# Kernel optimization log

Hardware: AMD Instinct MI355X
Metric: run time of the kernel (lower is better)

## Reference

```python
import jax, jax.numpy as jnp
import numpy as np


def _conv2d(x, w, b):
    # NCHW valid conv, kernel shape OIHW
    y = jax.lax.conv_general_dilated(x, w, (1, 1), 'VALID',
                                     dimension_numbers=('NCHW', 'OIHW', 'NCHW'))
    return y + b[None, :, None, None]


def _rgcn(x, src, dst, edge_type, root, rel, bias):
    # PyG RGCNConv: out_i = x_i @ root + bias + sum_r mean_{j in N_r(i)} x_j @ W_r
    # x: [B, N, F]; src/dst: [E]; rel: [R, F, F]
    out = x @ root + bias
    N = x.shape[1]
    for r in range(rel.shape[0]):  # small fixed relation count
        m = (edge_type == r).astype(x.dtype)                # [E]
        msg = (x @ rel[r])[:, src] * m[None, :, None]       # [B, E, F]
        agg = jnp.zeros_like(out).at[:, dst].add(msg)       # [B, N, F]
        cnt = jnp.zeros((N,), x.dtype).at[dst].add(m)       # per-node relation degree
        out = out + agg / jnp.clip(cnt, 1.0)[None, :, None]
    return out


def setup_inputs() -> dict:
    key = jax.random.key(0)
    ks = jax.random.split(key, 16)
    B, C, N, T = 16, 3, 3000, 50
    E, R, S, F = 96000, 3, 500, 43  # F = 2*20 + 3
    observation = jax.random.normal(ks[0], (B, C, N, T), jnp.float32)
    last_action = jax.random.uniform(ks[1], (B, S + 1), dtype=jnp.float32)
    edge_index = jax.random.randint(ks[2], (2, E), 0, N, jnp.int32)
    edge_type = jax.random.randint(ks[3], (E,), 0, R, jnp.int32)
    nodes_to_select = jnp.sort(jax.random.randint(ks[4], (S,), 0, N, jnp.int32))

    def w(k, shape, fan_in):
        return jax.random.normal(k, shape, jnp.float32) / np.sqrt(fan_in).astype(np.float32)

    params = dict(
        ws1=w(ks[5], (3, 3, 1, 3), 9), bs1=jnp.zeros(3, jnp.float32),
        ws2=w(ks[6], (20, 3, 1, 48), 144), bs2=jnp.zeros(20, jnp.float32),
        wm1=w(ks[7], (3, 3, 1, 21), 63), bm1=jnp.zeros(3, jnp.float32),
        wm2=w(ks[8], (20, 3, 1, 30), 90), bm2=jnp.zeros(20, jnp.float32),
        root1=w(ks[9], (F, F), F), rel1=w(ks[10], (R, F, F), F), bias1=jnp.zeros(F, jnp.float32),
        root2=w(ks[11], (F, F), F), rel2=w(ks[12], (R, F, F), F), bias2=jnp.zeros(F, jnp.float32),
        wf=w(ks[13], (1, 87, 1, 1), 87), bf=jnp.zeros(1, jnp.float32),
    )
    return {"observation": observation, "last_action": last_action,
            "edge_index": edge_index, "edge_type": edge_type,
            "nodes_to_select": nodes_to_select, **params}


def reference(observation, last_action, edge_index, edge_type, nodes_to_select,
              ws1, bs1, ws2, bs2, wm1, bm1, wm2, bm2,
              root1, rel1, bias1, root2, rel2, bias2, wf, bf):
    relu = jax.nn.relu
    B = observation.shape[0]
    last_stocks = last_action[:, 1:][:, None, :, None]                      # [B,1,S,1]
    short = relu(_conv2d(relu(_conv2d(observation, ws1, bs1)), ws2, bs2))   # [B,20,N,1]
    mid = relu(_conv2d(relu(_conv2d(observation, wm1, bm1)), wm2, bm2))     # [B,20,N,1]
    longf = relu(jnp.max(observation, axis=3, keepdims=True))               # [B,3,N,1]
    temporal = jnp.concatenate([short, mid, longf], axis=1)                 # [B,43,N,1]
    x = jnp.transpose(temporal[..., 0], (0, 2, 1))                          # [B,N,43]
    src, dst = edge_index[0], edge_index[1]
    h = jax.nn.leaky_relu(_rgcn(x, src, dst, edge_type, root1, rel1, bias1), 0.01)
    h = jax.nn.leaky_relu(_rgcn(h, src, dst, edge_type, root2, rel2, bias2), 0.01)
    graph_features = jnp.transpose(h, (0, 2, 1))[..., None]                 # [B,43,N,1]
    feats = jnp.concatenate([temporal, graph_features], axis=1)             # [B,86,N,1]
    feats = feats[:, :, nodes_to_select, :]                                 # [B,86,S,1]
    feats = jnp.concatenate([last_stocks, feats], axis=1)                   # [B,87,S,1]
    out = _conv2d(feats, wf, bf)                                            # [B,1,S,1]
    cash = jnp.zeros((B, 1, 1, 1), out.dtype)  # cash bias zeroed in mu()
    logits = jnp.concatenate([cash, out], axis=2)[:, 0, :, 0]               # [B,S+1]
    return jax.nn.softmax(logits, axis=-1)  # softmax_temperature = 1
```

## Files before the change

kernel.cpp:

```cpp
#include <hip/hip_runtime.h>
#include <math.h>

#define NB 16
#define NC 3
#define NN 3000
#define NT 50
#define NE 96000
#define NR 3
#define NS 500
#define NF 43
#define NFP 44
#define NBF (NB*NFP)
#define NBKT (NR*NN)
#define CAP 96

#define XT_OFF   0
#define H1_OFF   (XT_OFF + NN*NBF)
#define LG_OFF   (H1_OFF + NN*NBF)
#define INT_BASE (LG_OFF + NB*(NS+1))
#define CNT_OFF  0
#define EBUF_OFF (CNT_OFF + NBKT)

__global__ __launch_bounds__(256, 3) void k_front(
    const float* __restrict__ obs,
    const float* __restrict__ ws1, const float* __restrict__ bs1,
    const float* __restrict__ ws2, const float* __restrict__ bs2,
    const float* __restrict__ wm1, const float* __restrict__ bm1,
    const float* __restrict__ wm2, const float* __restrict__ bm2,
    float* __restrict__ x,
    const int* __restrict__ ei, const int* __restrict__ et,
    int* __restrict__ cnt, int* __restrict__ ebuf)
{
    __shared__ float sp[4][64][23];
    int tid = threadIdx.x;

    if (blockIdx.x >= 1500) {
        int e = (blockIdx.x - 1500) * 256 + tid;
        int bkt = et[e] * NN + ei[NE + e];
        int pos = atomicAdd(&cnt[bkt], 1);
        if (pos < CAP) ebuf[bkt * CAP + pos] = ei[e];
        return;
    }

    int wave = __builtin_amdgcn_readfirstlane(tid >> 6);
    int lane = tid & 63;

    if (blockIdx.x < 750) {
        int idx = blockIdx.x * 64 + lane;
        int b = idx / NN, n = idx - b * NN;
        float wS[3][14];
        int base = 12 * wave;
        #pragma unroll
        for (int c = 0; c < 3; ++c) {
            const float2* p2 = (const float2*)(obs + ((size_t)(b * NC + c) * NN + n) * NT + base);
            #pragma unroll
            for (int jj = 0; jj < 7; ++jj) {
                float2 u = p2[jj];
                wS[c][2 * jj] = u.x; wS[c][2 * jj + 1] = u.y;
            }
        }
        float acc[20];
        #pragma unroll
        for (int o = 0; o < 20; ++o) acc[o] = 0.f;
        #pragma unroll
        for (int j = 0; j < 12; ++j) {
            float y[3];
            #pragma unroll
            for (int c = 0; c < 3; ++c) {
                float s = bs1[c];
                #pragma unroll
                for (int i = 0; i < 3; ++i)
                    #pragma unroll
                    for (int k = 0; k < 3; ++k)
                        s = fmaf(wS[i][j + k], ws1[(c * 3 + i) * 3 + k], s);
                y[c] = fmaxf(s, 0.f);
            }
            int gt = base + j;
            #pragma unroll
            for (int o = 0; o < 20; ++o) {
                float a = acc[o];
                #pragma unroll
                for (int c = 0; c < 3; ++c)
                    a = fmaf(y[c], ws2[(o * 3 + c) * 48 + gt], a);
                acc[o] = a;
            }
        }
        #pragma unroll
        for (int o = 0; o < 20; ++o) sp[wave][lane][o] = acc[o];
        __syncthreads();
        #pragma unroll
        for (int q = 0; q < 5; ++q) {
            int item = q * 256 + tid;
            int node = item / 20, o = item - node * 20;
            int g = blockIdx.x * 64 + node;
            int bb = g / NN, nn = g - bb * NN;
            float s = ((sp[0][node][o] + sp[1][node][o]) +
                       (sp[2][node][o] + sp[3][node][o])) + bs2[o];
            x[(size_t)nn * NBF + bb * NFP + o] = fmaxf(s, 0.f);
        }
        return;
    }

    {
        int idx = (blockIdx.x - 750) * 64 + lane;
        int b = idx / NN, n = idx - b * NN;
        int mbase = (wave < 3) ? 8 * wave : 24;
        int nld   = (wave < 3) ? 14 : 13;
        const float* orow = obs + ((size_t)b * NC * NN + n) * NT + mbase;

        float s[3][8];
        #pragma unroll
        for (int c = 0; c < 3; ++c)
            #pragma unroll
            for (int t = 0; t < 8; ++t) s[c][t] = bm1[c];
        float cmax[3];
        float wA[28], wB[28];

        #define LOADW(buf, ch)                                                  \
        {                                                                       \
            const float2* p2 = (const float2*)(orow + (size_t)(ch) * NN * NT);  \
            _Pragma("unroll")                                                   \
            for (int jj = 0; jj < 14; ++jj) {                                   \
                if (jj < nld) {                                                 \
                    float2 u = p2[jj];                                          \
                    buf[2 * jj] = u.x; buf[2 * jj + 1] = u.y;                   \
                } else { buf[2 * jj] = 0.f; buf[2 * jj + 1] = 0.f; }            \
            }                                                                   \
        }
        #define COMPW(buf, ii)                                                  \
        {                                                                       \
            float m = buf[0];                                                   \
            _Pragma("unroll")                                                   \
            for (int t = 1; t < 28; ++t) m = fmaxf(m, buf[t]);                  \
            cmax[ii] = m;                                                       \
            _Pragma("unroll")                                                   \
            for (int c = 0; c < 3; ++c)                                         \
                _Pragma("unroll")                                               \
                for (int t = 0; t < 8; ++t) {                                   \
                    float a = s[c][t];                                          \
                    _Pragma("unroll")                                           \
                    for (int k = 0; k < 21; ++k)                                \
                        a = fmaf(buf[t + k], wm1[(c * 3 + (ii)) * 21 + k], a);  \
                    s[c][t] = a;                                                \
                }                                                               \
        }

        LOADW(wA, 0)
        LOADW(wB, 1)
        COMPW(wA, 0)
        LOADW(wA, 2)
        COMPW(wB, 1)
        COMPW(wA, 2)
        #undef LOADW
        #undef COMPW

        float acc[20];
        #pragma unroll
        for (int o = 0; o < 20; ++o) acc[o] = 0.f;
        int cntM = (wave < 3) ? 8 : 6;
        #pragma unroll
        for (int j = 0; j < 8; ++j) {
            if (j < cntM) {
                float y0 = fmaxf(s[0][j], 0.f);
                float y1 = fmaxf(s[1][j], 0.f);
                float y2 = fmaxf(s[2][j], 0.f);
                int gt = mbase + j;
                #pragma unroll
                for (int o = 0; o < 20; ++o) {
                    float a = acc[o];
                    a = fmaf(y0, wm2[(o * 3 + 0) * 30 + gt], a);
                    a = fmaf(y1, wm2[(o * 3 + 1) * 30 + gt], a);
                    a = fmaf(y2, wm2[(o * 3 + 2) * 30 + gt], a);
                    acc[o] = a;
                }
            }
        }
        #pragma unroll
        for (int o = 0; o < 20; ++o) sp[wave][lane][o] = acc[o];
        #pragma unroll
        for (int c = 0; c < 3; ++c) sp[wave][lane][20 + c] = cmax[c];
    }
    __syncthreads();
    #pragma unroll
    for (int q = 0; q < 6; ++q) {
        int item = q * 256 + tid;
        if (item < 1472) {
            int node = item / 23, o = item - node * 23;
            int g = (blockIdx.x - 750) * 64 + node;
            int bb = g / NN, nn = g - bb * NN;
            size_t row = (size_t)nn * NBF + bb * NFP;
            if (o < 20) {
                float s = ((sp[0][node][o] + sp[1][node][o]) +
                           (sp[2][node][o] + sp[3][node][o])) + bm2[o];
                x[row + 20 + o] = fmaxf(s, 0.f);
            } else {
                float m = fmaxf(fmaxf(sp[0][node][o], sp[1][node][o]),
                                fmaxf(sp[2][node][o], sp[3][node][o]));
                x[row + 40 + (o - 20)] = fmaxf(m, 0.f);
            }
        }
    }
}

template<bool LEAKY, bool SEL>
__global__ __launch_bounds__(256) void k_rgcn(
    const float* __restrict__ in, const float* __restrict__ xsrc,
    const int* __restrict__ cnt, const int* __restrict__ ebuf,
    const int* __restrict__ sel,
    const float* __restrict__ root, const float* __restrict__ rel,
    const float* __restrict__ bias,
    const float* __restrict__ la, const float* __restrict__ wf,
    const float* __restrict__ bf,
    float* __restrict__ out)
{
    __shared__ float lrow[4][NBF];
    __shared__ float sP[8][4][NFP];

    int tid = threadIdx.x;
    int wave = __builtin_amdgcn_readfirstlane(tid >> 6);
    int lane = tid & 63;
    int i = blockIdx.x;
    int node = __builtin_amdgcn_readfirstlane(SEL ? sel[i] : i);

    const float* wbase = (wave == 0) ? root : (rel + (size_t)(wave - 1) * NF * NF);
    float wsl[43];
    #pragma unroll
    for (int j = 0; j < 43; ++j)
        wsl[j] = (lane < NF) ? wbase[j * NF + lane] : 0.f;

    if (wave == 3) {
        #pragma unroll
        for (int j = 0; j < 11; ++j) {
            float v = in[(size_t)node * NBF + j * 64 + lane];
            if (LEAKY) v = v >= 0.f ? v : 0.01f * v;
            lrow[0][j * 64 + lane] = v;
        }
    } else {
        int bkt = wave * NN + node;
        int cvr = __builtin_amdgcn_readfirstlane(cnt[bkt]);
        float ic = 1.0f / fmaxf((float)cvr, 1.0f);
        int cv = cvr > CAP ? CAP : cvr;
        const int* eb = ebuf + bkt * CAP;

        float acc[11];
        #pragma unroll
        for (int j = 0; j < 11; ++j) acc[j] = 0.f;

        for (int e = 0; e < cv; e += 4) {
            int4 q = *(const int4*)(eb + e);
            int m = cv - e;
            {
                const float* p = in + (size_t)__builtin_amdgcn_readfirstlane(q.x) * NBF;
                #pragma unroll
                for (int j = 0; j < 11; ++j) {
                    float v = p[j * 64 + lane];
                    if (LEAKY) v = v >= 0.f ? v : 0.01f * v;
                    acc[j] += v;
                }
            }
            if (m > 1) {
                const float* p = in + (size_t)__builtin_amdgcn_readfirstlane(q.y) * NBF;
                #pragma unroll
                for (int j = 0; j < 11; ++j) {
                    float v = p[j * 64 + lane];
                    if (LEAKY) v = v >= 0.f ? v : 0.01f * v;
                    acc[j] += v;
                }
            }
            if (m > 2) {
                const float* p = in + (size_t)__builtin_amdgcn_readfirstlane(q.z) * NBF;
                #pragma unroll
                for (int j = 0; j < 11; ++j) {
                    float v = p[j * 64 + lane];
                    if (LEAKY) v = v >= 0.f ? v : 0.01f * v;
                    acc[j] += v;
                }
            }
            if (m > 3) {
                const float* p = in + (size_t)__builtin_amdgcn_readfirstlane(q.w) * NBF;
                #pragma unroll
                for (int j = 0; j < 11; ++j) {
                    float v = p[j * 64 + lane];
                    if (LEAKY) v = v >= 0.f ? v : 0.01f * v;
                    acc[j] += v;
                }
            }
        }
        #pragma unroll
        for (int j = 0; j < 11; ++j) lrow[wave + 1][j * 64 + lane] = acc[j] * ic;
    }
    __syncthreads();

    for (int h = 0; h < 2; ++h) {
        #pragma unroll
        for (int rr = 0; rr < 8; ++rr) {
            int b = h * 8 + rr;
            const float4* a4 = (const float4*)&lrow[wave][b * NFP];
            float a0 = 0.f, a1 = 0.f, a2 = 0.f, a3 = 0.f;
            #pragma unroll
            for (int c = 0; c < 10; ++c) {
                float4 v = a4[c];
                a0 = fmaf(v.x, wsl[4 * c], a0);
                a1 = fmaf(v.y, wsl[4 * c + 1], a1);
                a2 = fmaf(v.z, wsl[4 * c + 2], a2);
                a3 = fmaf(v.w, wsl[4 * c + 3], a3);
            }
            {
                float4 v = a4[10];
                a0 = fmaf(v.x, wsl[40], a0);
                a1 = fmaf(v.y, wsl[41], a1);
                a2 = fmaf(v.z, wsl[42], a2);
            }
            if (lane < NF) sP[rr][wave][lane] = (a0 + a1) + (a2 + a3);
        }
        __syncthreads();

        int r0 = 2 * wave, r1 = 2 * wave + 1;
        int b0 = h * 8 + r0, b1 = h * 8 + r1;
        if (!SEL) {
            if (lane < NF) {
                float bi_ = bias[lane];
                float s0 = ((sP[r0][0][lane] + sP[r0][1][lane]) +
                            (sP[r0][2][lane] + sP[r0][3][lane])) + bi_;
                float s1 = ((sP[r1][0][lane] + sP[r1][1][lane]) +
                            (sP[r1][2][lane] + sP[r1][3][lane])) + bi_;
                out[(size_t)i * NBF + b0 * NFP + lane] = s0;
                out[(size_t)i * NBF + b1 * NFP + lane] = s1;
            }
        } else {
            float p0 = 0.f, p1 = 0.f;
            if (lane < NF) {
                float bi_ = bias[lane];
                float s0 = ((sP[r0][0][lane] + sP[r0][1][lane]) +
                            (sP[r0][2][lane] + sP[r0][3][lane])) + bi_;
                float s1 = ((sP[r1][0][lane] + sP[r1][1][lane]) +
                            (sP[r1][2][lane] + sP[r1][3][lane])) + bi_;
                s0 = s0 >= 0.f ? s0 : 0.01f * s0;
                s1 = s1 >= 0.f ? s1 : 0.01f * s1;
                float x0 = xsrc[(size_t)node * NBF + b0 * NFP + lane];
                float x1 = xsrc[(size_t)node * NBF + b1 * NFP + lane];
                p0 = fmaf(wf[44 + lane], s0, wf[1 + lane] * x0);
                p1 = fmaf(wf[44 + lane], s1, wf[1 + lane] * x1);
            }
            #pragma unroll
            for (int o = 32; o > 0; o >>= 1) {
                p0 += __shfl_down(p0, o);
                p1 += __shfl_down(p1, o);
            }
            if (lane == 0) {
                out[(size_t)b0 * (NS + 1) + 1 + i] =
                    p0 + bf[0] + wf[0] * la[b0 * (NS + 1) + 1 + i];
                out[(size_t)b1 * (NS + 1) + 1 + i] =
                    p1 + bf[0] + wf[0] * la[b1 * (NS + 1) + 1 + i];
            }
        }
        __syncthreads();
    }
}

__device__ inline float wred_max(float v) {
    #pragma unroll
    for (int o = 32; o > 0; o >>= 1) v = fmaxf(v, __shfl_down(v, o));
    return v;
}
__device__ inline float wred_sum(float v) {
    #pragma unroll
    for (int o = 32; o > 0; o >>= 1) v += __shfl_down(v, o);
    return v;
}

__global__ __launch_bounds__(512) void k_softmax(
    const float* __restrict__ lg, float* __restrict__ out)
{
    __shared__ float sred[8];
    __shared__ float sbc[2];
    int b = blockIdx.x, tid = threadIdx.x;

    float val = -3.0e38f;
    if (tid <= NS) val = (tid == 0) ? 0.f : lg[(size_t)b * (NS + 1) + tid];

    float m = wred_max(val);
    if ((tid & 63) == 0) sred[tid >> 6] = m;
    __syncthreads();
    if (tid == 0) {
        float mm = sred[0];
        #pragma unroll
        for (int i = 1; i < 8; ++i) mm = fmaxf(mm, sred[i]);
        sbc[0] = mm;
    }
    __syncthreads();
    float mx = sbc[0];
    float e = (tid <= NS) ? expf(val - mx) : 0.f;
    float s = wred_sum(e);
    if ((tid & 63) == 0) sred[tid >> 6] = s;
    __syncthreads();
    if (tid == 0) {
        float t = 0.f;
        #pragma unroll
        for (int i = 0; i < 8; ++i) t += sred[i];
        sbc[1] = t;
    }
    __syncthreads();
    if (tid <= NS) out[(size_t)b * (NS + 1) + tid] = e / sbc[1];
}

extern "C" void kernel_launch(void* const* d_in, const int* in_sizes, int n_in,
                              void* d_out, int out_size, void* d_ws, size_t ws_size,
                              hipStream_t stream)
{
    const float* obs   = (const float*)d_in[0];
    const float* la    = (const float*)d_in[1];
    const int*   ei    = (const int*)d_in[2];
    const int*   et    = (const int*)d_in[3];
    const int*   nodes = (const int*)d_in[4];
    const float* ws1 = (const float*)d_in[5],  *bs1 = (const float*)d_in[6];
    const float* ws2 = (const float*)d_in[7],  *bs2 = (const float*)d_in[8];
    const float* wm1 = (const float*)d_in[9],  *bm1 = (const float*)d_in[10];
    const float* wm2 = (const float*)d_in[11], *bm2 = (const float*)d_in[12];
    const float* root1 = (const float*)d_in[13], *rel1 = (const float*)d_in[14], *bias1 = (const float*)d_in[15];
    const float* root2 = (const float*)d_in[16], *rel2 = (const float*)d_in[17], *bias2 = (const float*)d_in[18];
    const float* wf = (const float*)d_in[19], *bf = (const float*)d_in[20];

    float* wsp = (float*)d_ws;
    float* x   = wsp + XT_OFF;
    float* h1  = wsp + H1_OFF;
    float* lg  = wsp + LG_OFF;
    int*   ibase = (int*)(wsp + INT_BASE);
    int*   cnt   = ibase + CNT_OFF;
    int*   ebuf  = ibase + EBUF_OFF;

    hipMemsetAsync(cnt, 0, NBKT * sizeof(int), stream);

    k_front<<<1875, 256, 0, stream>>>(
        obs, ws1, bs1, ws2, bs2, wm1, bm1, wm2, bm2, x, ei, et, cnt, ebuf);

    k_rgcn<false, false><<<NN, 256, 0, stream>>>(
        x, nullptr, cnt, ebuf, nullptr, root1, rel1, bias1,
        nullptr, nullptr, nullptr, h1);

    k_rgcn<true, true><<<NS, 256, 0, stream>>>(
        h1, x, cnt, ebuf, nodes, root2, rel2, bias2,
        la, wf, bf, lg);

    k_softmax<<<NB, 512, 0, stream>>>(lg, (float*)d_out);
}
```

Measured before the change: 210.8 us.

## Stage observation tiles in LDS and spread edge gathers across all waves

The front kernel now loads each block's observation rows into shared memory with coalesced float2 loads, and the per-wave conv windows are read from there instead of from strided global rows. In the RGCN kernel all four waves now split every relation's neighbour list, striding by four and doing two gathers per iteration. Partial sums are combined with LDS atomics, and the mean normalisation is folded into the relation weight scale. This targets uncoalesced global loads and the load imbalance where one wave handled only the self row, at the cost of extra syncs, more LDS use and LDS atomic adds.

```diff
diff --git a/kernel.cpp b/kernel.cpp
--- a/kernel.cpp
+++ b/kernel.cpp
@@ -21,6 +21,8 @@
 #define CNT_OFF  0
 #define EBUF_OFF (CNT_OFF + NBKT)
 
+#define TS 51
+
 __global__ __launch_bounds__(256, 3) void k_front(
     const float* __restrict__ obs,
     const float* __restrict__ ws1, const float* __restrict__ bs1,
@@ -31,7 +33,7 @@
     const int* __restrict__ ei, const int* __restrict__ et,
     int* __restrict__ cnt, int* __restrict__ ebuf)
 {
-    __shared__ float sp[4][64][23];
+    __shared__ float smem[3 * 64 * TS];
     int tid = threadIdx.x;
 
     if (blockIdx.x >= 1500) {
@@ -44,21 +46,39 @@
 
     int wave = __builtin_amdgcn_readfirstlane(tid >> 6);
     int lane = tid & 63;
-
-    if (blockIdx.x < 750) {
-        int idx = blockIdx.x * 64 + lane;
-        int b = idx / NN, n = idx - b * NN;
+    bool isA = blockIdx.x < 750;
+    int idx0 = (isA ? blockIdx.x : blockIdx.x - 750) * 64;
+
+    #pragma unroll
+    for (int k = 0; k < 19; ++k) {
+        int f2 = k * 256 + tid;
+        if (f2 < 4800) {
+            int c = f2 / 1600;
+            int rem = f2 - c * 1600;
+            int nr = rem / 25;
+            int tp = rem - nr * 25;
+            int idx = idx0 + nr;
+            int b = idx / NN, n = idx - b * NN;
+            float2 u = *(const float2*)(obs + ((size_t)(b * NC + c) * NN + n) * NT + 2 * tp);
+            float* d = &smem[(c * 64 + nr) * TS + 2 * tp];
+            d[0] = u.x; d[1] = u.y;
+        }
+    }
+    __syncthreads();
+
+    #define SP(w, nd, o) smem[((w) * 64 + (nd)) * 23 + (o)]
+
+    if (isA) {
+        int base = 12 * wave;
         float wS[3][14];
-        int base = 12 * wave;
         #pragma unroll
         for (int c = 0; c < 3; ++c) {
-            const float2* p2 = (const float2*)(obs + ((size_t)(b * NC + c) * NN + n) * NT + base);
-            #pragma unroll
-            for (int jj = 0; jj < 7; ++jj) {
-                float2 u = p2[jj];
-                wS[c][2 * jj] = u.x; wS[c][2 * jj + 1] = u.y;
-            }
-        }
+            const float* sr = &smem[(c * 64 + lane) * TS + base];
+            #pragma unroll
+            for (int jj = 0; jj < 14; ++jj) wS[c][jj] = sr[jj];
+        }
+        __syncthreads();
+
         float acc[20];
         #pragma unroll
         for (int o = 0; o < 20; ++o) acc[o] = 0.f;
@@ -86,27 +106,24 @@
             }
         }
         #pragma unroll
-        for (int o = 0; o < 20; ++o) sp[wave][lane][o] = acc[o];
+        for (int o = 0; o < 20; ++o) SP(wave, lane, o) = acc[o];
         __syncthreads();
         #pragma unroll
         for (int q = 0; q < 5; ++q) {
             int item = q * 256 + tid;
             int node = item / 20, o = item - node * 20;
-            int g = blockIdx.x * 64 + node;
+            int g = idx0 + node;
             int bb = g / NN, nn = g - bb * NN;
-            float s = ((sp[0][node][o] + sp[1][node][o]) +
-                       (sp[2][node][o] + sp[3][node][o])) + bs2[o];
+            float s = ((SP(0, node, o) + SP(1, node, o)) +
+                       (SP(2, node, o) + SP(3, node, o))) + bs2[o];
             x[(size_t)nn * NBF + bb * NFP + o] = fmaxf(s, 0.f);
         }
         return;
     }
 
     {
-        int idx = (blockIdx.x - 750) * 64 + lane;
-        int b = idx / NN, n = idx - b * NN;
         int mbase = (wave < 3) ? 8 * wave : 24;
-        int nld   = (wave < 3) ? 14 : 13;
-        const float* orow = obs + ((size_t)b * NC * NN + n) * NT + mbase;
+        int nld   = (wave < 3) ? 28 : 26;
 
         float s[3][8];
         #pragma unroll
@@ -116,33 +133,29 @@
         float cmax[3];
         float wA[28], wB[28];
 
-        #define LOADW(buf, ch)                                                  \
-        {                                                                       \
-            const float2* p2 = (const float2*)(orow + (size_t)(ch) * NN * NT);  \
-            _Pragma("unroll")                                                   \
-            for (int jj = 0; jj < 14; ++jj) {                                   \
-                if (jj < nld) {                                                 \
-                    float2 u = p2[jj];                                          \
-                    buf[2 * jj] = u.x; buf[2 * jj + 1] = u.y;                   \
-                } else { buf[2 * jj] = 0.f; buf[2 * jj + 1] = 0.f; }            \
-            }                                                                   \
-        }
-        #define COMPW(buf, ii)                                                  \
-        {                                                                       \
-            float m = buf[0];                                                   \
-            _Pragma("unroll")                                                   \
-            for (int t = 1; t < 28; ++t) m = fmaxf(m, buf[t]);                  \
-            cmax[ii] = m;                                                       \
-            _Pragma("unroll")                                                   \
-            for (int c = 0; c < 3; ++c)                                         \
-                _Pragma("unroll")                                               \
-                for (int t = 0; t < 8; ++t) {                                   \
-                    float a = s[c][t];                                          \
-                    _Pragma("unroll")                                           \
-                    for (int k = 0; k < 21; ++k)                                \
-                        a = fmaf(buf[t + k], wm1[(c * 3 + (ii)) * 21 + k], a);  \
-                    s[c][t] = a;                                                \
-                }                                                               \
+        #define LOADW(buf, ch)                                              \
+        {                                                                   \
+            const float* sr = &smem[((ch) * 64 + lane) * TS + mbase];       \
+            _Pragma("unroll")                                               \
+            for (int t = 0; t < 28; ++t)                                    \
+                buf[t] = (t < nld) ? sr[t] : 0.f;                           \
+        }
+        #define COMPW(buf, ii)                                              \
+        {                                                                   \
+            float m = buf[0];                                               \
+            _Pragma("unroll")                                               \
+            for (int t = 1; t < 28; ++t) m = fmaxf(m, buf[t]);              \
+            cmax[ii] = m;                                                   \
+            _Pragma("unroll")                                               \
+            for (int c = 0; c < 3; ++c)                                     \
+                _Pragma("unroll")                                           \
+                for (int t = 0; t < 8; ++t) {                               \
+                    float a = s[c][t];                                      \
+                    _Pragma("unroll")                                       \
+                    for (int k = 0; k < 21; ++k)                            \
+                        a = fmaf(buf[t + k], wm1[(c * 3 + (ii)) * 21 + k], a); \
+                    s[c][t] = a;                                            \
+                }                                                           \
         }
 
         LOADW(wA, 0)
@@ -153,6 +166,7 @@
         COMPW(wA, 2)
         #undef LOADW
         #undef COMPW
+        __syncthreads();
 
         float acc[20];
         #pragma unroll
@@ -176,9 +190,9 @@
             }
         }
         #pragma unroll
-        for (int o = 0; o < 20; ++o) sp[wave][lane][o] = acc[o];
-        #pragma unroll
-        for (int c = 0; c < 3; ++c) sp[wave][lane][20 + c] = cmax[c];
+        for (int o = 0; o < 20; ++o) SP(wave, lane, o) = acc[o];
+        #pragma unroll
+        for (int c = 0; c < 3; ++c) SP(wave, lane, 20 + c) = cmax[c];
     }
     __syncthreads();
     #pragma unroll
@@ -186,20 +200,21 @@
         int item = q * 256 + tid;
         if (item < 1472) {
             int node = item / 23, o = item - node * 23;
-            int g = (blockIdx.x - 750) * 64 + node;
+            int g = idx0 + node;
             int bb = g / NN, nn = g - bb * NN;
             size_t row = (size_t)nn * NBF + bb * NFP;
             if (o < 20) {
-                float s = ((sp[0][node][o] + sp[1][node][o]) +
-                           (sp[2][node][o] + sp[3][node][o])) + bm2[o];
+                float s = ((SP(0, node, o) + SP(1, node, o)) +
+                           (SP(2, node, o) + SP(3, node, o))) + bm2[o];
                 x[row + 20 + o] = fmaxf(s, 0.f);
             } else {
-                float m = fmaxf(fmaxf(sp[0][node][o], sp[1][node][o]),
-                                fmaxf(sp[2][node][o], sp[3][node][o]));
+                float m = fmaxf(fmaxf(SP(0, node, o), SP(1, node, o)),
+                                fmaxf(SP(2, node, o), SP(3, node, o)));
                 x[row + 40 + (o - 20)] = fmaxf(m, 0.f);
             }
         }
     }
+    #undef SP
 }
 
 template<bool LEAKY, bool SEL>
@@ -222,73 +237,81 @@
     int i = blockIdx.x;
     int node = __builtin_amdgcn_readfirstlane(SEL ? sel[i] : i);
 
-    const float* wbase = (wave == 0) ? root : (rel + (size_t)(wave - 1) * NF * NF);
-    float wsl[43];
-    #pragma unroll
-    for (int j = 0; j < 43; ++j)
-        wsl[j] = (lane < NF) ? wbase[j * NF + lane] : 0.f;
-
-    if (wave == 3) {
-        #pragma unroll
-        for (int j = 0; j < 11; ++j) {
-            float v = in[(size_t)node * NBF + j * 64 + lane];
+    {
+        float* lz = &lrow[1][0];
+        #pragma unroll
+        for (int k = 0; k < 9; ++k) {
+            int t = k * 256 + tid;
+            if (t < 3 * NBF) lz[t] = 0.f;
+        }
+    }
+
+    int cv_[3]; float ic_[3];
+    #pragma unroll
+    for (int r = 0; r < 3; ++r) {
+        int c0 = __builtin_amdgcn_readfirstlane(cnt[r * NN + node]);
+        ic_[r] = 1.0f / fmaxf((float)c0, 1.0f);
+        cv_[r] = c0 > CAP ? CAP : c0;
+    }
+
+    #pragma unroll
+    for (int j = 0; j < 3; ++j) {
+        int sl = wave + 4 * j;
+        if (sl < 11) {
+            float v = in[(size_t)node * NBF + sl * 64 + lane];
             if (LEAKY) v = v >= 0.f ? v : 0.01f * v;
-            lrow[0][j * 64 + lane] = v;
-        }
-    } else {
-        int bkt = wave * NN + node;
-        int cvr = __builtin_amdgcn_readfirstlane(cnt[bkt]);
-        float ic = 1.0f / fmaxf((float)cvr, 1.0f);
-        int cv = cvr > CAP ? CAP : cvr;
-        const int* eb = ebuf + bkt * CAP;
-
-        float acc[11];
-        #pragma unroll
-        for (int j = 0; j < 11; ++j) acc[j] = 0.f;
-
-        for (int e = 0; e < cv; e += 4) {
-            int4 q = *(const int4*)(eb + e);
-            int m = cv - e;
-            {
-                const float* p = in + (size_t)__builtin_amdgcn_readfirstlane(q.x) * NBF;
+            lrow[0][sl * 64 + lane] = v;
+        }
+    }
+    __syncthreads();
+
+    #pragma unroll
+    for (int r = 0; r < 3; ++r) {
+        int cv = cv_[r];
+        if (cv > wave) {
+            const int* eb = ebuf + (size_t)(r * NN + node) * CAP;
+            float acc[11];
+            #pragma unroll
+            for (int j = 0; j < 11; ++j) acc[j] = 0.f;
+            int e = wave;
+            for (; e + 4 < cv; e += 8) {
+                int i0 = __builtin_amdgcn_readfirstlane(eb[e]);
+                int i1 = __builtin_amdgcn_readfirstlane(eb[e + 4]);
+                const float* p0 = in + (size_t)i0 * NBF;
+                const float* p1 = in + (size_t)i1 * NBF;
                 #pragma unroll
                 for (int j = 0; j < 11; ++j) {
-                    float v = p[j * 64 + lane];
+                    float va = p0[j * 64 + lane];
+                    float vb = p1[j * 64 + lane];
+                    if (LEAKY) {
+                        va = va >= 0.f ? va : 0.01f * va;
+                        vb = vb >= 0.f ? vb : 0.01f * vb;
+                    }
+                    acc[j] += va + vb;
+                }
+            }
+            if (e < cv) {
+                int i0 = __builtin_amdgcn_readfirstlane(eb[e]);
+                const float* p0 = in + (size_t)i0 * NBF;
+                #pragma unroll
+                for (int j = 0; j < 11; ++j) {
+                    float v = p0[j * 64 + lane];
                     if (LEAKY) v = v >= 0.f ? v : 0.01f * v;
                     acc[j] += v;
                 }
             }
-            if (m > 1) {
-                const float* p = in + (size_t)__builtin_amdgcn_readfirstlane(q.y) * NBF;
-                #pragma unroll
-                for (int j = 0; j < 11; ++j) {
-                    float v = p[j * 64 + lane];
-                    if (LEAKY) v = v >= 0.f ? v : 0.01f * v;
-                    acc[j] += v;
-                }
-            }
-            if (m > 2) {
-                const float* p = in + (size_t)__builtin_amdgcn_readfirstlane(q.z) * NBF;
-                #pragma unroll
-                for (int j = 0; j < 11; ++j) {
-                    float v = p[j * 64 + lane];
-                    if (LEAKY) v = v >= 0.f ? v : 0.01f * v;
-                    acc[j] += v;
-                }
-            }
-            if (m > 3) {
-                const float* p = in + (size_t)__builtin_amdgcn_readfirstlane(q.w) * NBF;
-                #pragma unroll
-                for (int j = 0; j < 11; ++j) {
-                    float v = p[j * 64 + lane];
-                    if (LEAKY) v = v >= 0.f ? v : 0.01f * v;
-                    acc[j] += v;
-                }
-            }
-        }
-        #pragma unroll
-        for (int j = 0; j < 11; ++j) lrow[wave + 1][j * 64 + lane] = acc[j] * ic;
-    }
+            #pragma unroll
+            for (int j = 0; j < 11; ++j)
+                atomicAdd(&lrow[r + 1][j * 64 + lane], acc[j]);
+        }
+    }
+
+    const float* wbase = (wave == 0) ? root : (rel + (size_t)(wave - 1) * NF * NF);
+    float wscale = (wave == 0) ? 1.0f : ic_[wave - 1];
+    float wsl[43];
+    #pragma unroll
+    for (int j = 0; j < 43; ++j)
+        wsl[j] = ((lane < NF) ? wbase[j * NF + lane] : 0.f) * wscale;
     __syncthreads();
 
     for (int h = 0; h < 2; ++h) {
```

After: 364.9 us. 1.73x slower.

## Split RGCN blocks by batch half, vectorize gathers and prefetch edge indices

Applied to the files above, without the earlier changes.

Each RGCN block now handles one node and half of the batch (8 of 16), doubling the grid to expose more parallelism. Blocks are ordered so the two halves of a group of four nodes sit near each other in launch order. Neighbour-row gathers now use float4 loads, and the first 24 edge indices are prefetched into scalar registers so the gather loop issues loads back to back. The trade-off is that weights and edge indices are loaded twice per node, and register pressure rises from the prefetch array.

```diff
diff --git a/kernel.cpp b/kernel.cpp
--- a/kernel.cpp
+++ b/kernel.cpp
@@ -13,6 +13,9 @@
 #define NBF (NB*NFP)
 #define NBKT (NR*NN)
 #define CAP 96
+#define PREF 24
+#define NHB 8
+#define NHF (NHB*NFP)
 
 #define XT_OFF   0
 #define H1_OFF   (XT_OFF + NN*NBF)
@@ -213,14 +216,19 @@
     const float* __restrict__ bf,
     float* __restrict__ out)
 {
-    __shared__ float lrow[4][NBF];
-    __shared__ float sP[8][4][NFP];
+    __shared__ __align__(16) float lrow[4][NHF];
+    __shared__ float sP[NHB][4][NFP];
 
     int tid = threadIdx.x;
     int wave = __builtin_amdgcn_readfirstlane(tid >> 6);
     int lane = tid & 63;
-    int i = blockIdx.x;
-    int node = __builtin_amdgcn_readfirstlane(SEL ? sel[i] : i);
+
+    int bid = blockIdx.x;
+    int g = bid >> 3, r = bid & 7;
+    int half = (r >> 2) & 1;
+    int idx = g * 4 + (r & 3);
+    int node = __builtin_amdgcn_readfirstlane(SEL ? sel[idx] : idx);
+    const float* inh = in + (size_t)node * NBF + half * NHF;
 
     const float* wbase = (wave == 0) ? root : (rel + (size_t)(wave - 1) * NF * NF);
     float wsl[43];
@@ -229,132 +237,148 @@
         wsl[j] = (lane < NF) ? wbase[j * NF + lane] : 0.f;
 
     if (wave == 3) {
-        #pragma unroll
-        for (int j = 0; j < 11; ++j) {
-            float v = in[(size_t)node * NBF + j * 64 + lane];
-            if (LEAKY) v = v >= 0.f ? v : 0.01f * v;
-            lrow[0][j * 64 + lane] = v;
+        const float4* p4 = (const float4*)inh;
+        float4 v0 = p4[lane];
+        if (LEAKY) {
+            v0.x = v0.x >= 0.f ? v0.x : 0.01f * v0.x;
+            v0.y = v0.y >= 0.f ? v0.y : 0.01f * v0.y;
+            v0.z = v0.z >= 0.f ? v0.z : 0.01f * v0.z;
+            v0.w = v0.w >= 0.f ? v0.w : 0.01f * v0.w;
+        }
+        *(float4*)&lrow[0][4 * lane] = v0;
+        if (lane < 24) {
+            float4 v1 = p4[64 + lane];
+            if (LEAKY) {
+                v1.x = v1.x >= 0.f ? v1.x : 0.01f * v1.x;
+                v1.y = v1.y >= 0.f ? v1.y : 0.01f * v1.y;
+                v1.z = v1.z >= 0.f ? v1.z : 0.01f * v1.z;
+                v1.w = v1.w >= 0.f ? v1.w : 0.01f * v1.w;
+            }
+            *(float4*)&lrow[0][4 * (64 + lane)] = v1;
         }
     } else {
         int bkt = wave * NN + node;
         int cvr = __builtin_amdgcn_readfirstlane(cnt[bkt]);
         float ic = 1.0f / fmaxf((float)cvr, 1.0f);
         int cv = cvr > CAP ? CAP : cvr;
-        const int* eb = ebuf + bkt * CAP;
-
-        float acc[11];
-        #pragma unroll
-        for (int j = 0; j < 11; ++j) acc[j] = 0.f;
-
-        for (int e = 0; e < cv; e += 4) {
-            int4 q = *(const int4*)(eb + e);
-            int m = cv - e;
-            {
-                const float* p = in + (size_t)__builtin_amdgcn_readfirstlane(q.x) * NBF;
-                #pragma unroll
-                for (int j = 0; j < 11; ++j) {
-                    float v = p[j * 64 + lane];
-                    if (LEAKY) v = v >= 0.f ? v : 0.01f * v;
-                    acc[j] += v;
-                }
-            }
-            if (m > 1) {
-                const float* p = in + (size_t)__builtin_amdgcn_readfirstlane(q.y) * NBF;
-                #pragma unroll
-                for (int j = 0; j < 11; ++j) {
-                    float v = p[j * 64 + lane];
-                    if (LEAKY) v = v >= 0.f ? v : 0.01f * v;
-                    acc[j] += v;
-                }
-            }
-            if (m > 2) {
-                const float* p = in + (size_t)__builtin_amdgcn_readfirstlane(q.z) * NBF;
-                #pragma unroll
-                for (int j = 0; j < 11; ++j) {
-                    float v = p[j * 64 + lane];
-                    if (LEAKY) v = v >= 0.f ? v : 0.01f * v;
-                    acc[j] += v;
-                }
-            }
-            if (m > 3) {
-                const float* p = in + (size_t)__builtin_amdgcn_readfirstlane(q.w) * NBF;
-                #pragma unroll
-                for (int j = 0; j < 11; ++j) {
-                    float v = p[j * 64 + lane];
-                    if (LEAKY) v = v >= 0.f ? v : 0.01f * v;
-                    acc[j] += v;
-                }
-            }
-        }
-        #pragma unroll
-        for (int j = 0; j < 11; ++j) lrow[wave + 1][j * 64 + lane] = acc[j] * ic;
-    }
-    __syncthreads();
-
-    for (int h = 0; h < 2; ++h) {
-        #pragma unroll
-        for (int rr = 0; rr < 8; ++rr) {
-            int b = h * 8 + rr;
-            const float4* a4 = (const float4*)&lrow[wave][b * NFP];
-            float a0 = 0.f, a1 = 0.f, a2 = 0.f, a3 = 0.f;
-            #pragma unroll
-            for (int c = 0; c < 10; ++c) {
-                float4 v = a4[c];
-                a0 = fmaf(v.x, wsl[4 * c], a0);
-                a1 = fmaf(v.y, wsl[4 * c + 1], a1);
-                a2 = fmaf(v.z, wsl[4 * c + 2], a2);
-                a3 = fmaf(v.w, wsl[4 * c + 3], a3);
-            }
-            {
-                float4 v = a4[10];
-                a0 = fmaf(v.x, wsl[40], a0);
-                a1 = fmaf(v.y, wsl[41], a1);
-                a2 = fmaf(v.z, wsl[42], a2);
-            }
-            if (lane < NF) sP[rr][wave][lane] = (a0 + a1) + (a2 + a3);
-        }
-        __syncthreads();
-
-        int r0 = 2 * wave, r1 = 2 * wave + 1;
-        int b0 = h * 8 + r0, b1 = h * 8 + r1;
-        if (!SEL) {
-            if (lane < NF) {
-                float bi_ = bias[lane];
-                float s0 = ((sP[r0][0][lane] + sP[r0][1][lane]) +
-                            (sP[r0][2][lane] + sP[r0][3][lane])) + bi_;
-                float s1 = ((sP[r1][0][lane] + sP[r1][1][lane]) +
-                            (sP[r1][2][lane] + sP[r1][3][lane])) + bi_;
-                out[(size_t)i * NBF + b0 * NFP + lane] = s0;
-                out[(size_t)i * NBF + b1 * NFP + lane] = s1;
-            }
-        } else {
-            float p0 = 0.f, p1 = 0.f;
-            if (lane < NF) {
-                float bi_ = bias[lane];
-                float s0 = ((sP[r0][0][lane] + sP[r0][1][lane]) +
-                            (sP[r0][2][lane] + sP[r0][3][lane])) + bi_;
-                float s1 = ((sP[r1][0][lane] + sP[r1][1][lane]) +
-                            (sP[r1][2][lane] + sP[r1][3][lane])) + bi_;
-                s0 = s0 >= 0.f ? s0 : 0.01f * s0;
-                s1 = s1 >= 0.f ? s1 : 0.01f * s1;
-                float x0 = xsrc[(size_t)node * NBF + b0 * NFP + lane];
-                float x1 = xsrc[(size_t)node * NBF + b1 * NFP + lane];
-                p0 = fmaf(wf[44 + lane], s0, wf[1 + lane] * x0);
-                p1 = fmaf(wf[44 + lane], s1, wf[1 + lane] * x1);
-            }
-            #pragma unroll
-            for (int o = 32; o > 0; o >>= 1) {
-                p0 += __shfl_down(p0, o);
-                p1 += __shfl_down(p1, o);
-            }
-            if (lane == 0) {
-                out[(size_t)b0 * (NS + 1) + 1 + i] =
-                    p0 + bf[0] + wf[0] * la[b0 * (NS + 1) + 1 + i];
-                out[(size_t)b1 * (NS + 1) + 1 + i] =
-                    p1 + bf[0] + wf[0] * la[b1 * (NS + 1) + 1 + i];
-            }
-        }
-        __syncthreads();
+        const int* eb = ebuf + (size_t)bkt * CAP;
+
+        int id[PREF];
+        #pragma unroll
+        for (int k = 0; k < PREF / 4; ++k) {
+            int4 q = *(const int4*)(eb + 4 * k);
+            id[4 * k + 0] = __builtin_amdgcn_readfirstlane(q.x);
+            id[4 * k + 1] = __builtin_amdgcn_readfirstlane(q.y);
+            id[4 * k + 2] = __builtin_amdgcn_readfirstlane(q.z);
+            id[4 * k + 3] = __builtin_amdgcn_readfirstlane(q.w);
+        }
+
+        float4 a0 = {0.f, 0.f, 0.f, 0.f};
+        float4 a1 = {0.f, 0.f, 0.f, 0.f};
+
+        #define GATHER(PTR)                                                  \
+        {                                                                    \
+            const float4* p = (const float4*)(PTR);                          \
+            float4 v0 = p[lane];                                             \
+            if (LEAKY) {                                                     \
+                v0.x = v0.x >= 0.f ? v0.x : 0.01f * v0.x;                    \
+                v0.y = v0.y >= 0.f ? v0.y : 0.01f * v0.y;                    \
+                v0.z = v0.z >= 0.f ? v0.z : 0.01f * v0.z;                    \
+                v0.w = v0.w >= 0.f ? v0.w : 0.01f * v0.w;                    \
+            }                                                                \
+            a0.x += v0.x; a0.y += v0.y; a0.z += v0.z; a0.w += v0.w;          \
+            if (lane < 24) {                                                 \
+                float4 v1 = p[64 + lane];                                    \
+                if (LEAKY) {                                                 \
+                    v1.x = v1.x >= 0.f ? v1.x : 0.01f * v1.x;                \
+                    v1.y = v1.y >= 0.f ? v1.y : 0.01f * v1.y;                \
+                    v1.z = v1.z >= 0.f ? v1.z : 0.01f * v1.z;                \
+                    v1.w = v1.w >= 0.f ? v1.w : 0.01f * v1.w;                \
+                }                                                            \
+                a1.x += v1.x; a1.y += v1.y; a1.z += v1.z; a1.w += v1.w;      \
+            }                                                                \
+        }
+
+        #pragma unroll
+        for (int e = 0; e < PREF; ++e) {
+            if (e < cv) GATHER(in + (size_t)id[e] * NBF + half * NHF)
+        }
+        for (int e = PREF; e < cv; ++e) {
+            int i0 = __builtin_amdgcn_readfirstlane(eb[e]);
+            GATHER(in + (size_t)i0 * NBF + half * NHF)
+        }
+        #undef GATHER
+
+        float* dst = &lrow[wave + 1][0];
+        a0.x *= ic; a0.y *= ic; a0.z *= ic; a0.w *= ic;
+        *(float4*)&dst[4 * lane] = a0;
+        if (lane < 24) {
+            a1.x *= ic; a1.y *= ic; a1.z *= ic; a1.w *= ic;
+            *(float4*)&dst[4 * (64 + lane)] = a1;
+        }
+    }
+    __syncthreads();
+
+    #pragma unroll
+    for (int rr = 0; rr < NHB; ++rr) {
+        const float4* a4 = (const float4*)&lrow[wave][rr * NFP];
+        float a0 = 0.f, a1 = 0.f, a2 = 0.f, a3 = 0.f;
+        #pragma unroll
+        for (int c = 0; c < 10; ++c) {
+            float4 v = a4[c];
+            a0 = fmaf(v.x, wsl[4 * c], a0);
+            a1 = fmaf(v.y, wsl[4 * c + 1], a1);
+            a2 = fmaf(v.z, wsl[4 * c + 2], a2);
+            a3 = fmaf(v.w, wsl[4 * c + 3], a3);
+        }
+        {
+            float4 v = a4[10];
+            a0 = fmaf(v.x, wsl[40], a0);
+            a1 = fmaf(v.y, wsl[41], a1);
+            a2 = fmaf(v.z, wsl[42], a2);
+        }
+        if (lane < NF) sP[rr][wave][lane] = (a0 + a1) + (a2 + a3);
+    }
+    __syncthreads();
+
+    int r0 = 2 * wave, r1 = 2 * wave + 1;
+    int b0 = half * NHB + r0, b1 = half * NHB + r1;
+    if (!SEL) {
+        if (lane < NF) {
+            float bi_ = bias[lane];
+            float s0 = ((sP[r0][0][lane] + sP[r0][1][lane]) +
+                        (sP[r0][2][lane] + sP[r0][3][lane])) + bi_;
+            float s1 = ((sP[r1][0][lane] + sP[r1][1][lane]) +
+                        (sP[r1][2][lane] + sP[r1][3][lane])) + bi_;
+            out[(size_t)idx * NBF + b0 * NFP + lane] = s0;
+            out[(size_t)idx * NBF + b1 * NFP + lane] = s1;
+        }
+    } else {
+        float p0 = 0.f, p1 = 0.f;
+        if (lane < NF) {
+            float bi_ = bias[lane];
+            float s0 = ((sP[r0][0][lane] + sP[r0][1][lane]) +
+                        (sP[r0][2][lane] + sP[r0][3][lane])) + bi_;
+            float s1 = ((sP[r1][0][lane] + sP[r1][1][lane]) +
+                        (sP[r1][2][lane] + sP[r1][3][lane])) + bi_;
+            s0 = s0 >= 0.f ? s0 : 0.01f * s0;
+            s1 = s1 >= 0.f ? s1 : 0.01f * s1;
+            float x0 = xsrc[(size_t)node * NBF + b0 * NFP + lane];
+            float x1 = xsrc[(size_t)node * NBF + b1 * NFP + lane];
+            p0 = fmaf(wf[44 + lane], s0, wf[1 + lane] * x0);
+            p1 = fmaf(wf[44 + lane], s1, wf[1 + lane] * x1);
+        }
+        #pragma unroll
+        for (int o = 32; o > 0; o >>= 1) {
+            p0 += __shfl_down(p0, o);
+            p1 += __shfl_down(p1, o);
+        }
+        if (lane == 0) {
+            out[(size_t)b0 * (NS + 1) + 1 + idx] =
+                p0 + bf[0] + wf[0] * la[b0 * (NS + 1) + 1 + idx];
+            out[(size_t)b1 * (NS + 1) + 1 + idx] =
+                p1 + bf[0] + wf[0] * la[b1 * (NS + 1) + 1 + idx];
+        }
     }
 }
 
@@ -434,11 +458,11 @@
     k_front<<<1875, 256, 0, stream>>>(
         obs, ws1, bs1, ws2, bs2, wm1, bm1, wm2, bm2, x, ei, et, cnt, ebuf);
 
-    k_rgcn<false, false><<<NN, 256, 0, stream>>>(
+    k_rgcn<false, false><<<NN * 2, 256, 0, stream>>>(
         x, nullptr, cnt, ebuf, nullptr, root1, rel1, bias1,
         nullptr, nullptr, nullptr, h1);
 
-    k_rgcn<true, true><<<NS, 256, 0, stream>>>(
+    k_rgcn<true, true><<<NS * 2, 256, 0, stream>>>(
         h1, x, cnt, ebuf, nodes, root2, rel2, bias2,
         la, wf, bf, lg);
 
```

Measured after the change: 213.6 us. No clear change (+1.3%).
